# Optimization experiments

Measured on AMD Instinct MI355X. Metric: run time of the kernel, lower is better.

The kernel has to match this reference:

```python
import jax, jax.numpy as jnp
import numpy as np

N = 50000    # nodes
E = 640000   # edges (avg degree ~12.8)
D = 128      # feature dim (input = hidden = output)
L = 3        # num_layers
BN_EPS = 1e-5


def setup_inputs() -> dict:
    key = jax.random.key(0)
    ks = jax.random.split(key, 6)
    x = jax.random.normal(ks[0], (N, D), dtype=jnp.float32)
    edge_index = jax.random.randint(ks[1], (2, E), 0, N, dtype=jnp.int32)
    s = 1.0 / np.sqrt(D)
    # Weights stored as (in, out); equivalent to torch Linear's x @ W.T with W:(out,in).
    W1 = jax.random.normal(ks[2], (L, D, D), dtype=jnp.float32) * s
    b1 = jnp.zeros((L, D), dtype=jnp.float32)
    gamma = jnp.ones((L, D), dtype=jnp.float32)   # BatchNorm weight
    beta = jnp.zeros((L, D), dtype=jnp.float32)   # BatchNorm bias
    W2 = jax.random.normal(ks[3], (L, D, D), dtype=jnp.float32) * s
    b2 = jnp.zeros((L, D), dtype=jnp.float32)
    return {"x": x, "W1": W1, "b1": b1, "gamma": gamma, "beta": beta,
            "W2": W2, "b2": b2, "edge_index": edge_index}


def reference(x, W1, b1, gamma, beta, W2, b2, edge_index):
    src = edge_index[0]
    dst = edge_index[1]
    h = x
    for i in range(L):
        # GINConv aggregation: sum of source-node features into destinations, eps=0
        agg = jax.ops.segment_sum(h[src], dst, num_segments=N)   # [N, D]
        z = h + agg                                              # (1+eps)*x + sum_j x_j
        # MLP: Linear -> BatchNorm1d (training stats) -> ReLU -> Linear
        z = z @ W1[i] + b1[i]
        mu = jnp.mean(z, axis=0)
        var = jnp.mean((z - mu) ** 2, axis=0)                    # biased var (torch BN)
        z = (z - mu) * jax.lax.rsqrt(var + BN_EPS) * gamma[i] + beta[i]
        z = jax.nn.relu(z)
        z = z @ W2[i] + b2[i]
        # inter-layer ReLU (dropout_rate=0 -> identity)
        h = jax.nn.relu(z) if i < L - 1 else z
    return h
```

## Files before the change

### kernel.cpp

```cpp
#include <hip/hip_runtime.h>

#define D 128
#define BN_EPS 1e-5f
#define ELLW 64
#define SGRP 8

typedef __bf16 bf16_t;
typedef __bf16 bf16x8 __attribute__((ext_vector_type(8)));
typedef __bf16 bf16x4 __attribute__((ext_vector_type(4)));
typedef __bf16 bf16x2 __attribute__((ext_vector_type(2)));
typedef float floatx4 __attribute__((ext_vector_type(4)));

__global__ void prep(const float* __restrict__ x, bf16_t* __restrict__ hb,
                     const float* __restrict__ W1, const float* __restrict__ W2,
                     bf16_t* __restrict__ Wsw, int* __restrict__ deg,
                     float* __restrict__ stats, int N, int n4) {
  int i = blockIdx.x * blockDim.x + threadIdx.x;
  if (i < n4) {
    float4 v = ((const float4*)x)[i];
    bf16x4 p;
    p[0] = (bf16_t)v.x; p[1] = (bf16_t)v.y; p[2] = (bf16_t)v.z; p[3] = (bf16_t)v.w;
    *(bf16x4*)(hb + (size_t)4 * i) = p;
  }
  if (i < N) deg[i] = 0;
  if (i < 3 * SGRP * 256) stats[i] = 0.f;
  if (i < 6 * 16384) {
    int mat = i >> 14;
    int kn = i & 16383;
    int k = kn >> 7;
    int n = kn & 127;
    const float* Wm = (mat < 3) ? (W1 + (size_t)mat * 16384)
                                : (W2 + (size_t)(mat - 3) * 16384);
    float v = Wm[kn];
    int f = ((n >> 4) << 2) | (k >> 5);
    int ln = (((k >> 3) & 3) << 4) | (n & 15);
    int j = k & 7;
    Wsw[(size_t)mat * 16384 + ((f << 6) + ln) * 8 + j] = (bf16_t)v;
  }
}

__global__ void ell_fill(const int* __restrict__ src, const int* __restrict__ dst,
                         int* __restrict__ deg, int* __restrict__ ell, int E) {
  int e = blockIdx.x * blockDim.x + threadIdx.x;
  if (e < E) {
    int d = dst[e];
    int slot = atomicAdd(&deg[d], 1);
    if (slot < ELLW) ell[(size_t)d * ELLW + slot] = src[e];
  }
}

__global__ __launch_bounds__(256) void aggregate(
    const bf16_t* __restrict__ h, bf16_t* __restrict__ z,
    const int* __restrict__ ell, const int* __restrict__ deg, int Nn) {
  int node = blockIdx.x * 8 + (threadIdx.x >> 5);
  if (node >= Nn) return;
  int s = threadIdx.x & 31;
  int off = s << 2;
  int dg = deg[node]; if (dg > ELLW) dg = ELLW;
  const int* nb = ell + (size_t)node * ELLW;

  bf16x4 sv = *(const bf16x4*)(h + (size_t)node * D + off);
  floatx4 A0 = {(float)sv[0], (float)sv[1], (float)sv[2], (float)sv[3]};
  floatx4 A1 = {0.f, 0.f, 0.f, 0.f};
  floatx4 A2 = {0.f, 0.f, 0.f, 0.f};
  floatx4 A3 = {0.f, 0.f, 0.f, 0.f};
  int e = 0;
  for (; e + 8 <= dg; e += 8) {
    int4 ia = *(const int4*)(nb + e);
    int4 ib = *(const int4*)(nb + e + 4);
    bf16x4 v0 = *(const bf16x4*)(h + (size_t)ia.x * D + off);
    bf16x4 v1 = *(const bf16x4*)(h + (size_t)ia.y * D + off);
    bf16x4 v2 = *(const bf16x4*)(h + (size_t)ia.z * D + off);
    bf16x4 v3 = *(const bf16x4*)(h + (size_t)ia.w * D + off);
    bf16x4 v4 = *(const bf16x4*)(h + (size_t)ib.x * D + off);
    bf16x4 v5 = *(const bf16x4*)(h + (size_t)ib.y * D + off);
    bf16x4 v6 = *(const bf16x4*)(h + (size_t)ib.z * D + off);
    bf16x4 v7 = *(const bf16x4*)(h + (size_t)ib.w * D + off);
#pragma unroll
    for (int j = 0; j < 4; ++j) {
      A0[j] += (float)v0[j];
      A1[j] += (float)v1[j];
      A2[j] += (float)v2[j];
      A3[j] += (float)v3[j];
      A0[j] += (float)v4[j];
      A1[j] += (float)v5[j];
      A2[j] += (float)v6[j];
      A3[j] += (float)v7[j];
    }
  }
  for (; e + 4 <= dg; e += 4) {
    int4 i4 = *(const int4*)(nb + e);
    bf16x4 v0 = *(const bf16x4*)(h + (size_t)i4.x * D + off);
    bf16x4 v1 = *(const bf16x4*)(h + (size_t)i4.y * D + off);
    bf16x4 v2 = *(const bf16x4*)(h + (size_t)i4.z * D + off);
    bf16x4 v3 = *(const bf16x4*)(h + (size_t)i4.w * D + off);
#pragma unroll
    for (int j = 0; j < 4; ++j) {
      A0[j] += (float)v0[j];
      A1[j] += (float)v1[j];
      A2[j] += (float)v2[j];
      A3[j] += (float)v3[j];
    }
  }
  for (; e < dg; ++e) {
    bf16x4 v = *(const bf16x4*)(h + (size_t)nb[e] * D + off);
#pragma unroll
    for (int j = 0; j < 4; ++j) A0[j] += (float)v[j];
  }
#pragma unroll
  for (int j = 0; j < 4; ++j) A0[j] += A1[j] + A2[j] + A3[j];
  bf16x4 o;
  o[0] = (bf16_t)A0[0]; o[1] = (bf16_t)A0[1];
  o[2] = (bf16_t)A0[2]; o[3] = (bf16_t)A0[3];
  *(bf16x4*)(z + (size_t)node * D + off) = o;
}

__global__ __launch_bounds__(256) void gemm1_stats(
    const bf16_t* __restrict__ Z, const bf16_t* __restrict__ Wsw1,
    const float* __restrict__ bias1, float* __restrict__ stats,
    int nStrips, int N) {
  __shared__ float sred[256];
  const int t = threadIdx.x;
  const int lane = t & 63;
  const int l15 = lane & 15;
  const int quad = lane >> 4;
  const int strip = blockIdx.x * 4 + (t >> 6);
  const bool active = strip < nStrips;

  sred[t] = 0.f;
  __syncthreads();

  bf16x8 a[4];
  const int row = strip * 16 + l15;
  if (active && row < N) {
#pragma unroll
    for (int kc = 0; kc < 4; ++kc)
      a[kc] = *(const bf16x8*)(Z + (size_t)row * D + kc * 32 + quad * 8);
  } else {
#pragma unroll
    for (int kc = 0; kc < 4; ++kc)
#pragma unroll
      for (int j = 0; j < 8; ++j) a[kc][j] = (bf16_t)0.f;
  }

  floatx4 acc[8];
#pragma unroll
  for (int nt = 0; nt < 8; ++nt) {
    float bv = bias1[nt * 16 + l15];
    acc[nt] = (floatx4){bv, bv, bv, bv};
  }
#pragma unroll
  for (int nt = 0; nt < 8; ++nt) {
#pragma unroll
    for (int kc = 0; kc < 4; ++kc) {
      bf16x8 b = *(const bf16x8*)(Wsw1 + (size_t)((nt * 4 + kc) * 64 + lane) * 8);
      acc[nt] = __builtin_amdgcn_mfma_f32_16x16x32_bf16(a[kc], b, acc[nt], 0, 0, 0);
    }
  }

  const int rowBase = strip * 16 + quad * 4;
#pragma unroll
  for (int nt = 0; nt < 8; ++nt) {
    int c = nt * 16 + l15;
    float s = 0.f, q = 0.f;
    if (active) {
#pragma unroll
      for (int r = 0; r < 4; ++r) {
        if (rowBase + r < N) {
          float v = acc[nt][r];
          s += v; q += v * v;
        }
      }
    }
    s += __shfl_xor(s, 16); s += __shfl_xor(s, 32);
    q += __shfl_xor(q, 16); q += __shfl_xor(q, 32);
    if (quad == 0) {
      atomicAdd(&sred[c], s);
      atomicAdd(&sred[128 + c], q);
    }
  }
  __syncthreads();
  atomicAdd(&stats[((blockIdx.x & (SGRP - 1)) << 8) + t], sred[t]);
}

__global__ __launch_bounds__(256) void mlp2r(
    const bf16_t* __restrict__ Z, const float* __restrict__ stats,
    const float* __restrict__ gamma, const float* __restrict__ beta,
    const bf16_t* __restrict__ Wsw1, const float* __restrict__ bias1,
    const bf16_t* __restrict__ Wsw2, const float* __restrict__ bias2,
    void* __restrict__ outp, int nStrips, int N, float invN,
    int relu_out, int fp32_out) {
  __shared__ bf16_t T[64][136];
  __shared__ float abL[256];
  const int t = threadIdx.x;
  const int wv = t >> 6;
  const int lane = t & 63;
  const int l15 = lane & 15;
  const int quad = lane >> 4;
  const int strip = blockIdx.x * 4 + wv;
  const bool active = strip < nStrips;

  if (t < 128) {
    float s0 = 0.f, q0 = 0.f;
#pragma unroll
    for (int g = 0; g < SGRP; ++g) {
      s0 += stats[(g << 8) + t];
      q0 += stats[(g << 8) + 128 + t];
    }
    float mu = s0 * invN;
    float var = fmaxf(q0 * invN - mu * mu, 0.f);
    float ai = gamma[t] * rsqrtf(var + BN_EPS);
    abL[t] = ai;
    abL[128 + t] = beta[t] - mu * ai;
  }

  bf16x8 a[4];
  const int row = strip * 16 + l15;
  if (active && row < N) {
#pragma unroll
    for (int kc = 0; kc < 4; ++kc)
      a[kc] = *(const bf16x8*)(Z + (size_t)row * D + kc * 32 + quad * 8);
  } else {
#pragma unroll
    for (int kc = 0; kc < 4; ++kc)
#pragma unroll
      for (int j = 0; j < 8; ++j) a[kc][j] = (bf16_t)0.f;
  }

  floatx4 acc[8];
#pragma unroll
  for (int nt = 0; nt < 8; ++nt) {
    float bv = bias1[nt * 16 + l15];
    acc[nt] = (floatx4){bv, bv, bv, bv};
  }
#pragma unroll
  for (int nt = 0; nt < 8; ++nt) {
#pragma unroll
    for (int kc = 0; kc < 4; ++kc) {
      bf16x8 b = *(const bf16x8*)(Wsw1 + (size_t)((nt * 4 + kc) * 64 + lane) * 8);
      acc[nt] = __builtin_amdgcn_mfma_f32_16x16x32_bf16(a[kc], b, acc[nt], 0, 0, 0);
    }
  }

  __syncthreads();

  float bnA[8], bnB[8];
#pragma unroll
  for (int nt = 0; nt < 8; ++nt) {
    int c = nt * 16 + l15;
    bnA[nt] = abL[c];
    bnB[nt] = abL[128 + c];
  }

  const int lr = wv * 16 + quad * 4;
#pragma unroll
  for (int nt = 0; nt < 8; ++nt) {
    int c = nt * 16 + l15;
#pragma unroll
    for (int r = 0; r < 4; ++r)
      T[lr + r][c] = (bf16_t)fmaxf(fmaf(acc[nt][r], bnA[nt], bnB[nt]), 0.f);
  }
  __syncthreads();

  bf16x8 a2[4];
#pragma unroll
  for (int kc = 0; kc < 4; ++kc)
    a2[kc] = *(const bf16x8*)&T[wv * 16 + l15][kc * 32 + quad * 8];

#pragma unroll
  for (int nt = 0; nt < 8; ++nt) {
    float bv = bias2[nt * 16 + l15];
    acc[nt] = (floatx4){bv, bv, bv, bv};
  }
#pragma unroll
  for (int nt = 0; nt < 8; ++nt) {
#pragma unroll
    for (int kc = 0; kc < 4; ++kc) {
      bf16x8 b = *(const bf16x8*)(Wsw2 + (size_t)((nt * 4 + kc) * 64 + lane) * 8);
      acc[nt] = __builtin_amdgcn_mfma_f32_16x16x32_bf16(a2[kc], b, acc[nt], 0, 0, 0);
    }
  }

  if (!active) return;
  const int rowBase = strip * 16 + quad * 4;
  if (fp32_out) {
    float* out = (float*)outp;
#pragma unroll
    for (int nt = 0; nt < 8; ++nt) {
      int c = nt * 16 + l15;
#pragma unroll
      for (int r = 0; r < 4; ++r) {
        int rw = rowBase + r;
        if (rw < N) {
          float v = acc[nt][r];
          if (relu_out) v = fmaxf(v, 0.f);
          out[(size_t)rw * D + c] = v;
        }
      }
    }
  } else {
    bf16_t* out = (bf16_t*)outp;
#pragma unroll
    for (int nt = 0; nt < 8; ++nt) {
      int c = nt * 16 + l15;
#pragma unroll
      for (int r = 0; r < 4; ++r) {
        int rw = rowBase + r;
        if (rw < N) {
          float v = acc[nt][r];
          if (relu_out) v = fmaxf(v, 0.f);
          out[(size_t)rw * D + c] = (bf16_t)v;
        }
      }
    }
  }
}

extern "C" void kernel_launch(void* const* d_in, const int* in_sizes, int n_in,
                              void* d_out, int out_size, void* d_ws, size_t ws_size,
                              hipStream_t stream) {
  const float* x     = (const float*)d_in[0];
  const float* W1    = (const float*)d_in[1];
  const float* b1    = (const float*)d_in[2];
  const float* gamma = (const float*)d_in[3];
  const float* beta  = (const float*)d_in[4];
  const float* W2    = (const float*)d_in[5];
  const float* b2    = (const float*)d_in[6];
  const int*   ei    = (const int*)d_in[7];

  const int N = in_sizes[0] / D;
  const int E = in_sizes[7] / 2;
  const int* src = ei;
  const int* dst = ei + E;

  char* ws = (char*)d_ws;
  size_t bufBytes = (size_t)N * D * sizeof(bf16_t);
  bf16_t* hb   = (bf16_t*)ws;
  bf16_t* zb   = (bf16_t*)(ws + bufBytes);
  int*    ell  = (int*)(ws + 2 * bufBytes);
  int*    deg  = (int*)((char*)ell + (size_t)N * ELLW * sizeof(int));
  float*  stats = (float*)((char*)deg + (size_t)N * sizeof(int));
  bf16_t* Wsw  = (bf16_t*)(stats + 3 * SGRP * 256);

  const int n4 = N * D / 4;
  const int prepBlocks = (n4 + 255) / 256;
  const int eb = (E + 255) / 256;
  const int aggBlocks = (N + 7) / 8;
  const int nStrips = (N + 15) / 16;
  const int gemmBlocks = (nStrips + 3) / 4;
  const float invN = 1.f / (float)N;

  prep<<<prepBlocks, 256, 0, stream>>>(x, hb, W1, W2, Wsw, deg, stats, N, n4);
  ell_fill<<<eb, 256, 0, stream>>>(src, dst, deg, ell, E);

  for (int i = 0; i < 3; ++i) {
    float* st = stats + (size_t)i * SGRP * 256;
    aggregate<<<aggBlocks, 256, 0, stream>>>(hb, zb, ell, deg, N);
    gemm1_stats<<<gemmBlocks, 256, 0, stream>>>(
        zb, Wsw + (size_t)i * 16384, b1 + (size_t)i * D, st, nStrips, N);
    void* Ob = (i == 2) ? d_out : (void*)hb;
    mlp2r<<<gemmBlocks, 256, 0, stream>>>(
        zb, st, gamma + (size_t)i * D, beta + (size_t)i * D,
        Wsw + (size_t)i * 16384, b1 + (size_t)i * D,
        Wsw + (size_t)(i + 3) * 16384, b2 + (size_t)i * D,
        Ob, nStrips, N, invN, (i < 2) ? 1 : 0, (i == 2) ? 1 : 0);
  }
}
```

Baseline: 297.3 us.

## Fuse neighbor aggregation with first GEMM and BN stats kernel

Merges the aggregation kernel and the gemm1_stats kernel into one kernel. Each 256-thread block aggregates 64 nodes into a shared-memory tile, then runs the MFMA GEMM and BatchNorm statistics from that tile instead of re-reading Z from global memory. Z is still written out for the later mlp2r pass. This removes one launch and one global read of Z per layer. In exchange each block's aggregation runs serially over 8 passes with a block barrier, which may cut the latency hiding available for the irregular gathers.

```diff
diff --git a/kernel.cpp b/kernel.cpp
--- a/kernel.cpp
+++ b/kernel.cpp
@@ -49,99 +49,96 @@
   }
 }
 
-__global__ __launch_bounds__(256) void aggregate(
+__global__ __launch_bounds__(256) void agg_gemm1(
     const bf16_t* __restrict__ h, bf16_t* __restrict__ z,
-    const int* __restrict__ ell, const int* __restrict__ deg, int Nn) {
-  int node = blockIdx.x * 8 + (threadIdx.x >> 5);
-  if (node >= Nn) return;
-  int s = threadIdx.x & 31;
-  int off = s << 2;
-  int dg = deg[node]; if (dg > ELLW) dg = ELLW;
-  const int* nb = ell + (size_t)node * ELLW;
-
-  bf16x4 sv = *(const bf16x4*)(h + (size_t)node * D + off);
-  floatx4 A0 = {(float)sv[0], (float)sv[1], (float)sv[2], (float)sv[3]};
-  floatx4 A1 = {0.f, 0.f, 0.f, 0.f};
-  floatx4 A2 = {0.f, 0.f, 0.f, 0.f};
-  floatx4 A3 = {0.f, 0.f, 0.f, 0.f};
-  int e = 0;
-  for (; e + 8 <= dg; e += 8) {
-    int4 ia = *(const int4*)(nb + e);
-    int4 ib = *(const int4*)(nb + e + 4);
-    bf16x4 v0 = *(const bf16x4*)(h + (size_t)ia.x * D + off);
-    bf16x4 v1 = *(const bf16x4*)(h + (size_t)ia.y * D + off);
-    bf16x4 v2 = *(const bf16x4*)(h + (size_t)ia.z * D + off);
-    bf16x4 v3 = *(const bf16x4*)(h + (size_t)ia.w * D + off);
-    bf16x4 v4 = *(const bf16x4*)(h + (size_t)ib.x * D + off);
-    bf16x4 v5 = *(const bf16x4*)(h + (size_t)ib.y * D + off);
-    bf16x4 v6 = *(const bf16x4*)(h + (size_t)ib.z * D + off);
-    bf16x4 v7 = *(const bf16x4*)(h + (size_t)ib.w * D + off);
-#pragma unroll
-    for (int j = 0; j < 4; ++j) {
-      A0[j] += (float)v0[j];
-      A1[j] += (float)v1[j];
-      A2[j] += (float)v2[j];
-      A3[j] += (float)v3[j];
-      A0[j] += (float)v4[j];
-      A1[j] += (float)v5[j];
-      A2[j] += (float)v6[j];
-      A3[j] += (float)v7[j];
-    }
-  }
-  for (; e + 4 <= dg; e += 4) {
-    int4 i4 = *(const int4*)(nb + e);
-    bf16x4 v0 = *(const bf16x4*)(h + (size_t)i4.x * D + off);
-    bf16x4 v1 = *(const bf16x4*)(h + (size_t)i4.y * D + off);
-    bf16x4 v2 = *(const bf16x4*)(h + (size_t)i4.z * D + off);
-    bf16x4 v3 = *(const bf16x4*)(h + (size_t)i4.w * D + off);
-#pragma unroll
-    for (int j = 0; j < 4; ++j) {
-      A0[j] += (float)v0[j];
-      A1[j] += (float)v1[j];
-      A2[j] += (float)v2[j];
-      A3[j] += (float)v3[j];
-    }
-  }
-  for (; e < dg; ++e) {
-    bf16x4 v = *(const bf16x4*)(h + (size_t)nb[e] * D + off);
-#pragma unroll
-    for (int j = 0; j < 4; ++j) A0[j] += (float)v[j];
-  }
-#pragma unroll
-  for (int j = 0; j < 4; ++j) A0[j] += A1[j] + A2[j] + A3[j];
-  bf16x4 o;
-  o[0] = (bf16_t)A0[0]; o[1] = (bf16_t)A0[1];
-  o[2] = (bf16_t)A0[2]; o[3] = (bf16_t)A0[3];
-  *(bf16x4*)(z + (size_t)node * D + off) = o;
-}
-
-__global__ __launch_bounds__(256) void gemm1_stats(
-    const bf16_t* __restrict__ Z, const bf16_t* __restrict__ Wsw1,
-    const float* __restrict__ bias1, float* __restrict__ stats,
-    int nStrips, int N) {
+    const int* __restrict__ ell, const int* __restrict__ deg,
+    const bf16_t* __restrict__ Wsw1, const float* __restrict__ bias1,
+    float* __restrict__ stats, int N) {
+  __shared__ bf16_t T[64][136];
   __shared__ float sred[256];
   const int t = threadIdx.x;
+  const int wv = t >> 6;
   const int lane = t & 63;
+  const int half = lane >> 5;
+  const int s = lane & 31;
+  const int off = s << 2;
   const int l15 = lane & 15;
   const int quad = lane >> 4;
-  const int strip = blockIdx.x * 4 + (t >> 6);
-  const bool active = strip < nStrips;
+  const int rowBaseBlk = blockIdx.x * 64;
 
   sred[t] = 0.f;
+
+  for (int p = 0; p < 8; ++p) {
+    const int lrow = wv * 16 + (p << 1) + half;
+    const int node = rowBaseBlk + lrow;
+    floatx4 A0 = {0.f, 0.f, 0.f, 0.f};
+    floatx4 A1 = {0.f, 0.f, 0.f, 0.f};
+    floatx4 A2 = {0.f, 0.f, 0.f, 0.f};
+    floatx4 A3 = {0.f, 0.f, 0.f, 0.f};
+    if (node < N) {
+      int dg = deg[node]; if (dg > ELLW) dg = ELLW;
+      const int* nb = ell + (size_t)node * ELLW;
+      bf16x4 sv = *(const bf16x4*)(h + (size_t)node * D + off);
+      A0[0] = (float)sv[0]; A0[1] = (float)sv[1];
+      A0[2] = (float)sv[2]; A0[3] = (float)sv[3];
+      int e = 0;
+      for (; e + 8 <= dg; e += 8) {
+        int4 ia = *(const int4*)(nb + e);
+        int4 ib = *(const int4*)(nb + e + 4);
+        bf16x4 v0 = *(const bf16x4*)(h + (size_t)ia.x * D + off);
+        bf16x4 v1 = *(const bf16x4*)(h + (size_t)ia.y * D + off);
+        bf16x4 v2 = *(const bf16x4*)(h + (size_t)ia.z * D + off);
+        bf16x4 v3 = *(const bf16x4*)(h + (size_t)ia.w * D + off);
+        bf16x4 v4 = *(const bf16x4*)(h + (size_t)ib.x * D + off);
+        bf16x4 v5 = *(const bf16x4*)(h + (size_t)ib.y * D + off);
+        bf16x4 v6 = *(const bf16x4*)(h + (size_t)ib.z * D + off);
+        bf16x4 v7 = *(const bf16x4*)(h + (size_t)ib.w * D + off);
+#pragma unroll
+        for (int j = 0; j < 4; ++j) {
+          A0[j] += (float)v0[j];
+          A1[j] += (float)v1[j];
+          A2[j] += (float)v2[j];
+          A3[j] += (float)v3[j];
+          A0[j] += (float)v4[j];
+          A1[j] += (float)v5[j];
+          A2[j] += (float)v6[j];
+          A3[j] += (float)v7[j];
+        }
+      }
+      for (; e + 4 <= dg; e += 4) {
+        int4 i4 = *(const int4*)(nb + e);
+        bf16x4 v0 = *(const bf16x4*)(h + (size_t)i4.x * D + off);
+        bf16x4 v1 = *(const bf16x4*)(h + (size_t)i4.y * D + off);
+        bf16x4 v2 = *(const bf16x4*)(h + (size_t)i4.z * D + off);
+        bf16x4 v3 = *(const bf16x4*)(h + (size_t)i4.w * D + off);
+#pragma unroll
+        for (int j = 0; j < 4; ++j) {
+          A0[j] += (float)v0[j];
+          A1[j] += (float)v1[j];
+          A2[j] += (float)v2[j];
+          A3[j] += (float)v3[j];
+        }
+      }
+      for (; e < dg; ++e) {
+        bf16x4 v = *(const bf16x4*)(h + (size_t)nb[e] * D + off);
+#pragma unroll
+        for (int j = 0; j < 4; ++j) A0[j] += (float)v[j];
+      }
+    }
+#pragma unroll
+    for (int j = 0; j < 4; ++j) A0[j] += A1[j] + A2[j] + A3[j];
+    bf16x4 o;
+    o[0] = (bf16_t)A0[0]; o[1] = (bf16_t)A0[1];
+    o[2] = (bf16_t)A0[2]; o[3] = (bf16_t)A0[3];
+    *(bf16x4*)&T[lrow][off] = o;
+    if (node < N) *(bf16x4*)(z + (size_t)node * D + off) = o;
+  }
   __syncthreads();
 
   bf16x8 a[4];
-  const int row = strip * 16 + l15;
-  if (active && row < N) {
-#pragma unroll
-    for (int kc = 0; kc < 4; ++kc)
-      a[kc] = *(const bf16x8*)(Z + (size_t)row * D + kc * 32 + quad * 8);
-  } else {
-#pragma unroll
-    for (int kc = 0; kc < 4; ++kc)
-#pragma unroll
-      for (int j = 0; j < 8; ++j) a[kc][j] = (bf16_t)0.f;
-  }
+#pragma unroll
+  for (int kc = 0; kc < 4; ++kc)
+    a[kc] = *(const bf16x8*)&T[wv * 16 + l15][kc * 32 + quad * 8];
 
   floatx4 acc[8];
 #pragma unroll
@@ -158,24 +155,22 @@
     }
   }
 
-  const int rowBase = strip * 16 + quad * 4;
+  const int rowBase = rowBaseBlk + wv * 16 + quad * 4;
 #pragma unroll
   for (int nt = 0; nt < 8; ++nt) {
     int c = nt * 16 + l15;
-    float s = 0.f, q = 0.f;
-    if (active) {
-#pragma unroll
-      for (int r = 0; r < 4; ++r) {
-        if (rowBase + r < N) {
-          float v = acc[nt][r];
-          s += v; q += v * v;
-        }
-      }
-    }
-    s += __shfl_xor(s, 16); s += __shfl_xor(s, 32);
+    float sum = 0.f, q = 0.f;
+#pragma unroll
+    for (int r = 0; r < 4; ++r) {
+      if (rowBase + r < N) {
+        float v = acc[nt][r];
+        sum += v; q += v * v;
+      }
+    }
+    sum += __shfl_xor(sum, 16); sum += __shfl_xor(sum, 32);
     q += __shfl_xor(q, 16); q += __shfl_xor(q, 32);
     if (quad == 0) {
-      atomicAdd(&sred[c], s);
+      atomicAdd(&sred[c], sum);
       atomicAdd(&sred[128 + c], q);
     }
   }
@@ -345,7 +340,7 @@
   const int n4 = N * D / 4;
   const int prepBlocks = (n4 + 255) / 256;
   const int eb = (E + 255) / 256;
-  const int aggBlocks = (N + 7) / 8;
+  const int fusedBlocks = (N + 63) / 64;
   const int nStrips = (N + 15) / 16;
   const int gemmBlocks = (nStrips + 3) / 4;
   const float invN = 1.f / (float)N;
@@ -355,9 +350,8 @@
 
   for (int i = 0; i < 3; ++i) {
     float* st = stats + (size_t)i * SGRP * 256;
-    aggregate<<<aggBlocks, 256, 0, stream>>>(hb, zb, ell, deg, N);
-    gemm1_stats<<<gemmBlocks, 256, 0, stream>>>(
-        zb, Wsw + (size_t)i * 16384, b1 + (size_t)i * D, st, nStrips, N);
+    agg_gemm1<<<fusedBlocks, 256, 0, stream>>>(
+        hb, zb, ell, deg, Wsw + (size_t)i * 16384, b1 + (size_t)i * D, st, N);
     void* Ob = (i == 2) ? d_out : (void*)hb;
     mlp2r<<<gemmBlocks, 256, 0, stream>>>(
         zb, st, gamma + (size_t)i * D, beta + (size_t)i * D,
```

Measured after the change: 309.7 us. 4.2% more time.
